# Performance work log

Hardware: AMD Instinct MI355X
Metric: run time of the kernel (lower is better)

## Reference

```python
import jax, jax.numpy as jnp
import numpy as np

NUM_LAYERS = 24
LN_EPS = 1e-5


def setup_inputs() -> dict:
    key = jax.random.key(0)
    ks = jax.random.split(key, 8)
    B, S = 256, 8192
    x = jax.random.uniform(ks[0], (B, S, 5), dtype=jnp.float32)
    # per-layer LayerNorm(4) params (torch default init: weight=1, bias=0; use
    # randomized values so the gather is non-trivial)
    ln_w = 1.0 + 0.1 * jax.random.normal(ks[1], (NUM_LAYERS, 4), dtype=jnp.float32)
    ln_b = 0.1 * jax.random.normal(ks[2], (NUM_LAYERS, 4), dtype=jnp.float32)
    # MLP 5 -> 64 -> 32 -> 1 (dropout inactive in eval mode)
    W1 = jax.random.normal(ks[3], (64, 5), dtype=jnp.float32) / np.sqrt(5)
    b1 = jnp.zeros((64,), dtype=jnp.float32)
    W2 = jax.random.normal(ks[4], (32, 64), dtype=jnp.float32) / np.sqrt(64)
    b2 = jnp.zeros((32,), dtype=jnp.float32)
    W3 = jax.random.normal(ks[5], (1, 32), dtype=jnp.float32) / np.sqrt(32)
    b3 = jnp.zeros((1,), dtype=jnp.float32)
    return {"x": x, "ln_w": ln_w, "ln_b": ln_b, "W1": W1, "b1": b1,
            "W2": W2, "b2": b2, "W3": W3, "b3": b3}


def reference(x, ln_w, ln_b, W1, b1, W2, b2, W3, b3):
    B, S, _ = x.shape
    x_flat = x.reshape(-1, 5)                      # [N, 5]
    layer_pos = x_flat[:, -1]                      # [N]
    layer_ids = jnp.clip((layer_pos * NUM_LAYERS).astype(jnp.int32), 0, NUM_LAYERS - 1)
    feats = x_flat[:, :4]                          # [N, 4]
    # vectorized per-token LayerNorm: gather per-token gamma/beta by layer id
    mean = jnp.mean(feats, axis=-1, keepdims=True)
    var = jnp.mean(jnp.square(feats - mean), axis=-1, keepdims=True)  # biased, as torch LN
    normed = (feats - mean) * jax.lax.rsqrt(var + LN_EPS)
    normed = normed * ln_w[layer_ids] + ln_b[layer_ids]               # [N, 4]
    x_norm = jnp.concatenate([normed, layer_pos[:, None]], axis=1)    # [N, 5]
    h = jax.nn.relu(x_norm @ W1.T + b1)            # [N, 64]
    h = jax.nn.relu(h @ W2.T + b2)                 # [N, 32]
    scores = h @ W3.T + b3                         # [N, 1]
    return scores.reshape(B, S)
```

## Files before the change

### kernel.cpp

```cpp
#include <hip/hip_runtime.h>
#include <stdint.h>

#define NUM_LAYERS 24
#define LN_EPS 1e-5f
#define N_ROWS (256 * 8192)
#define ROWS_PER_ITER 128
#define NUM_ITERS (N_ROWS / ROWS_PER_ITER)
#define NUM_BLOCKS 2048

typedef __attribute__((ext_vector_type(4)))  uint32_t u32x4;
typedef __attribute__((ext_vector_type(16))) float    f32x16;
typedef __attribute__((ext_vector_type(2)))  float    f32x2;
typedef __attribute__((ext_vector_type(2)))  __fp16   h16x2;

__device__ __forceinline__ uint32_t pk_f16_rtz(float lo, float hi) {
    h16x2 v = __builtin_amdgcn_cvt_pkrtz(lo, hi);
    uint32_t u; __builtin_memcpy(&u, &v, 4);
    return u;
}
__device__ __forceinline__ uint32_t pk_f16_rne(float lo, float hi) {
    __fp16 a = (__fp16)lo, b = (__fp16)hi;
    uint16_t ua, ub;
    __builtin_memcpy(&ua, &a, 2); __builtin_memcpy(&ub, &b, 2);
    return (uint32_t)ua | ((uint32_t)ub << 16);
}
__device__ __forceinline__ uint32_t pk_relu_f16(uint32_t d) {
    h16x2 v; __builtin_memcpy(&v, &d, 4);
    h16x2 z = {(__fp16)0.0f, (__fp16)0.0f};
    v = __builtin_elementwise_max(v, z);
    uint32_t u; __builtin_memcpy(&u, &v, 4);
    return u;
}

__device__ __forceinline__ u32x4 make_frag(uint32_t d0, uint32_t d1,
                                           uint32_t d2, uint32_t d3) {
    u32x4 f; f.x = d0; f.y = d1; f.z = d2; f.w = d3;
    return f;
}

__device__ __forceinline__ void mfma_l1(f32x16& d0, f32x16& d1,
                                        f32x16& d2, f32x16& d3,
                                        const u32x4& a0, const u32x4& a1,
                                        const u32x4& b0, const u32x4& b1) {
    asm("s_nop 2\n\t"
        "v_mfma_f32_32x32x16_f16 %0, %4, %6, 0\n\t"
        "v_mfma_f32_32x32x16_f16 %1, %5, %6, 0\n\t"
        "v_mfma_f32_32x32x16_f16 %2, %4, %7, 0\n\t"
        "v_mfma_f32_32x32x16_f16 %3, %5, %7, 0"
        : "=&v"(d0), "=&v"(d1), "=&v"(d2), "=&v"(d3)
        : "v"(a0), "v"(a1), "v"(b0), "v"(b1));
}
__device__ __forceinline__ void mfma_l2(f32x16& c0, f32x16& c1, const f32x16& cinit,
                                        const u32x4& w0, const u32x4& w1,
                                        const u32x4& w2, const u32x4& w3,
                                        const u32x4& h00, const u32x4& h01,
                                        const u32x4& h02, const u32x4& h03,
                                        const u32x4& h10, const u32x4& h11,
                                        const u32x4& h12, const u32x4& h13) {
    asm("s_nop 2\n\t"
        "v_mfma_f32_32x32x16_f16 %0, %3, %7, %2\n\t"
        "v_mfma_f32_32x32x16_f16 %1, %3, %11, %2\n\t"
        "v_mfma_f32_32x32x16_f16 %0, %4, %8, %0\n\t"
        "v_mfma_f32_32x32x16_f16 %1, %4, %12, %1\n\t"
        "v_mfma_f32_32x32x16_f16 %0, %5, %9, %0\n\t"
        "v_mfma_f32_32x32x16_f16 %1, %5, %13, %1\n\t"
        "v_mfma_f32_32x32x16_f16 %0, %6, %10, %0\n\t"
        "v_mfma_f32_32x32x16_f16 %1, %6, %14, %1"
        : "=&v"(c0), "=&v"(c1)
        : "v"(cinit), "v"(w0), "v"(w1), "v"(w2), "v"(w3),
          "v"(h00), "v"(h01), "v"(h02), "v"(h03),
          "v"(h10), "v"(h11), "v"(h12), "v"(h13));
}
__device__ __forceinline__ void mfma_fence2(f32x16& c0, f32x16& c1) {
    asm volatile("s_nop 7\n\ts_nop 7\n\ts_nop 7" : "+v"(c0), "+v"(c1));
}
__device__ __forceinline__ void mfma_fence4(f32x16& c0, f32x16& c1,
                                            f32x16& c2, f32x16& c3) {
    asm volatile("s_nop 7\n\ts_nop 7\n\ts_nop 7"
                 : "+v"(c0), "+v"(c1), "+v"(c2), "+v"(c3));
}

__device__ __forceinline__ int sigma_k(int p) {
    int hh = (p >> 2) & 1;
    int base = (p & 31) - 4 * hh;
    int r = (base & 3) + 4 * (base >> 3);
    return 32 * (p >> 5) + 16 * (r >> 3) + 8 * hh + (r & 7);
}

__global__ __launch_bounds__(256, 3) void router_mfma(
    const float* __restrict__ x,
    const float* __restrict__ ln_w,
    const float* __restrict__ ln_b,
    const float* __restrict__ W1,
    const float* __restrict__ b1,
    const float* __restrict__ W2,
    const float* __restrict__ b2,
    const float* __restrict__ W3,
    const float* __restrict__ b3,
    float* __restrict__ out)
{
    __shared__ uint32_t s_a1[2 * 64 * 4];
    __shared__ uint32_t s_w2[4 * 64 * 4];
    __shared__ float    s_w3[8 * 64 * 2];
    __shared__ float    s_b2[8 * 64 * 2];
    __shared__ float    s_ln[8 * NUM_LAYERS];

    const int t = threadIdx.x;

    if (t < 8 * NUM_LAYERS) {
        const int q = t & 7, lid = t >> 3;
        s_ln[q * NUM_LAYERS + lid] =
            (q < 4) ? ln_w[lid * 4 + q] : ln_b[lid * 4 + (q - 4)];
    }
    if (t < 128) {
        const int mt = t >> 6, ln = t & 63;
        const int n32l = ln & 31, hl = ln >> 5;
        uint32_t d0 = 0, d1 = 0, d2 = 0;
        if (!hl) {
            const int k = sigma_k(mt * 32 + n32l);
            d0 = pk_f16_rne(W1[k * 5 + 0], W1[k * 5 + 1]);
            d1 = pk_f16_rne(W1[k * 5 + 2], W1[k * 5 + 3]);
            d2 = pk_f16_rne(W1[k * 5 + 4], b1[k]);
        }
        uint32_t* p = &s_a1[(mt * 64 + ln) * 4];
        p[0] = d0; p[1] = d1; p[2] = d2; p[3] = 0;
    }
    {
        const int kt = t >> 6, ln = t & 63;
        const int n32l = ln & 31, hl = ln >> 5;
        const float* wp = W2 + n32l * 64 + kt * 16 + hl * 8;
        const float4 lo = *(const float4*)(wp);
        const float4 hi = *(const float4*)(wp + 4);
        uint32_t* p = &s_w2[(kt * 64 + ln) * 4];
        p[0] = pk_f16_rne(lo.x, lo.y);
        p[1] = pk_f16_rne(lo.z, lo.w);
        p[2] = pk_f16_rne(hi.x, hi.y);
        p[3] = pk_f16_rne(hi.z, hi.w);
    }
#pragma unroll
    for (int e = t; e < 512; e += 256) {
        const int r2 = e >> 6, ln = e & 63;
        const int hl = ln >> 5;
        const int n = ((2 * r2) & 3) + 8 * (r2 >> 1) + 4 * hl;
        s_w3[e * 2 + 0] = W3[n];
        s_w3[e * 2 + 1] = W3[n + 1];
        s_b2[e * 2 + 0] = b2[n];
        s_b2[e * 2 + 1] = b2[n + 1];
    }
    __syncthreads();

    const int lane = t & 63;
    const int wid  = t >> 6;
    const int h    = lane >> 5;

    u32x4 a1f[2], w2f[4];
#pragma unroll
    for (int mt = 0; mt < 2; ++mt)
        a1f[mt] = *(const u32x4*)&s_a1[(mt * 64 + lane) * 4];
#pragma unroll
    for (int kt = 0; kt < 4; ++kt)
        w2f[kt] = *(const u32x4*)&s_w2[(kt * 64 + lane) * 4];

    f32x16 c2init;
    f32x2 w3p[8];
#pragma unroll
    for (int r2 = 0; r2 < 8; ++r2) {
        w3p[r2] = *(const f32x2*)&s_w3[(r2 * 64 + lane) * 2];
        const f32x2 bp = *(const f32x2*)&s_b2[(r2 * 64 + lane) * 2];
        c2init[2 * r2]     = bp.x;
        c2init[2 * r2 + 1] = bp.y;
    }
    const float b3v = b3[0];
    const f32x2 z2 = {0.0f, 0.0f};

    const int total_waves = NUM_BLOCKS * 4;
    const int w = blockIdx.x * 4 + wid;

    int it = w;
    {
        const float* p0 = x + (size_t)(it * ROWS_PER_ITER + lane) * 5;
        const float* p1 = x + (size_t)(it * ROWS_PER_ITER + 64 + lane) * 5;
        float4 c40 = *(const float4*)p0; float cl0 = p0[4];
        float4 c41 = *(const float4*)p1; float cl1 = p1[4];

        while (true) {
            const int nit = it + total_waves;
            const bool more = nit < NUM_ITERS;
            const size_t nb = (size_t)(more ? nit : it) * ROWS_PER_ITER;
            const float* n0 = x + (nb + lane) * 5;
            const float* n1 = x + (nb + 64 + lane) * 5;
            const float4 nv40 = *(const float4*)n0; const float nl0 = n0[4];
            const float4 nv41 = *(const float4*)n1; const float nl1 = n1[4];

            const int rowBase = it * ROWS_PER_ITER;

#pragma unroll
            for (int grp = 0; grp < 2; ++grp) {
                const float4 cv = grp ? c41 : c40;
                const float  cl = grp ? cl1 : cl0;
                const int gbase = rowBase + 64 * grp;

                int lid = (int)(cl * (float)NUM_LAYERS);
                lid = lid < 0 ? 0 : (lid > NUM_LAYERS - 1 ? NUM_LAYERS - 1 : lid);

                const float m  = (cv.x + cv.y + cv.z + cv.w) * 0.25f;
                const float d0 = cv.x - m, d1 = cv.y - m,
                            d2 = cv.z - m, d3 = cv.w - m;
                const float var = (d0 * d0 + d1 * d1 + d2 * d2 + d3 * d3) * 0.25f;
                const float r   = rsqrtf(var + LN_EPS);

                const float xn0 = fmaf(d0, r * s_ln[0 * 24 + lid], s_ln[4 * 24 + lid]);
                const float xn1 = fmaf(d1, r * s_ln[1 * 24 + lid], s_ln[5 * 24 + lid]);
                const float xn2 = fmaf(d2, r * s_ln[2 * 24 + lid], s_ln[6 * 24 + lid]);
                const float xn3 = fmaf(d3, r * s_ln[3 * 24 + lid], s_ln[7 * 24 + lid]);

                const uint32_t e0 = pk_f16_rtz(xn0, xn1);
                const uint32_t e1 = pk_f16_rtz(xn2, xn3);
                const uint32_t e2 = pk_f16_rtz(cl, 1.0f);
                const uint32_t x0 = __shfl_xor((int)e0, 32, 64);
                const uint32_t x1 = __shfl_xor((int)e1, 32, 64);
                const uint32_t x2 = __shfl_xor((int)e2, 32, 64);

                const u32x4 bf_t0 = make_frag(e0, e1, e2, 0u);
                const u32x4 bf_t1 = make_frag(x0, x1, x2, 0u);

                f32x16 c1a0, c1b0, c1a1, c1b1;
                mfma_l1(c1a0, c1b0, c1a1, c1b1, a1f[0], a1f[1], bf_t0, bf_t1);
                mfma_fence4(c1a0, c1b0, c1a1, c1b1);

                u32x4 h1f0[4], h1f1[4];
#pragma unroll
                for (int kt = 0; kt < 4; ++kt) {
                    const f32x16& c1 = (kt < 2) ? c1a0 : c1b0;
                    const int roff = 8 * (kt & 1);
                    uint32_t dw[4];
#pragma unroll
                    for (int d = 0; d < 4; ++d)
                        dw[d] = pk_relu_f16(
                            pk_f16_rtz(c1[roff + 2 * d], c1[roff + 2 * d + 1]));
                    h1f0[kt] = make_frag(dw[0], dw[1], dw[2], dw[3]);
                }
#pragma unroll
                for (int kt = 0; kt < 4; ++kt) {
                    const f32x16& c1 = (kt < 2) ? c1a1 : c1b1;
                    const int roff = 8 * (kt & 1);
                    uint32_t dw[4];
#pragma unroll
                    for (int d = 0; d < 4; ++d)
                        dw[d] = pk_relu_f16(
                            pk_f16_rtz(c1[roff + 2 * d], c1[roff + 2 * d + 1]));
                    h1f1[kt] = make_frag(dw[0], dw[1], dw[2], dw[3]);
                }

                f32x16 c2_0, c2_1;
                mfma_l2(c2_0, c2_1, c2init,
                        w2f[0], w2f[1], w2f[2], w2f[3],
                        h1f0[0], h1f0[1], h1f0[2], h1f0[3],
                        h1f1[0], h1f1[1], h1f1[2], h1f1[3]);
                mfma_fence2(c2_0, c2_1);

                f32x2 acc0 = z2, acc1 = z2;
#pragma unroll
                for (int r2 = 0; r2 < 8; ++r2) {
                    f32x2 v0 = {c2_0[2 * r2], c2_0[2 * r2 + 1]};
                    f32x2 v1 = {c2_1[2 * r2], c2_1[2 * r2 + 1]};
                    v0 = __builtin_elementwise_max(v0, z2);
                    v1 = __builtin_elementwise_max(v1, z2);
                    acc0 = v0 * w3p[r2] + acc0;
                    acc1 = v1 * w3p[r2] + acc1;
                }
                float q0 = acc0.x + acc0.y;
                float q1 = acc1.x + acc1.y;
                q0 += __shfl_xor(q0, 32, 64);
                q1 += __shfl_xor(q1, 32, 64);

                out[gbase + lane] = (h ? q1 : q0) + b3v;
            }

            if (!more) break;
            it = nit;
            c40 = nv40; cl0 = nl0; c41 = nv41; cl1 = nl1;
        }
    }
}

extern "C" void kernel_launch(void* const* d_in, const int* in_sizes, int n_in,
                              void* d_out, int out_size, void* d_ws, size_t ws_size,
                              hipStream_t stream) {
    const float* x    = (const float*)d_in[0];
    const float* ln_w = (const float*)d_in[1];
    const float* ln_b = (const float*)d_in[2];
    const float* W1   = (const float*)d_in[3];
    const float* b1   = (const float*)d_in[4];
    const float* W2   = (const float*)d_in[5];
    const float* b2   = (const float*)d_in[6];
    const float* W3   = (const float*)d_in[7];
    const float* b3   = (const float*)d_in[8];
    float* out = (float*)d_out;

    router_mfma<<<NUM_BLOCKS, 256, 0, stream>>>(x, ln_w, ln_b, W1, b1, W2, b2,
                                                W3, b3, out);
}
```

Baseline: 107.2 us.

## Replace persistent prefetch loop with one-shot 256-row-per-wave batched processing

Drops the grid-stride loop that prefetched the next 128-row tile. Each wave now handles exactly 256 rows: it issues all four 64-row loads up front, runs LayerNorm and fragment packing for all four groups, then runs the MFMA chain per group. Launch bounds fall from 3 to 2 blocks per CU to allow the extra registers this needs. More memory-level parallelism per wave comes at the cost of lower occupancy and no overlap across tiles.

After: 106.6 us. About the same (-0.5%).

```diff
diff --git a/kernel.cpp b/kernel.cpp
--- a/kernel.cpp
+++ b/kernel.cpp
@@ -4,8 +4,6 @@
 #define NUM_LAYERS 24
 #define LN_EPS 1e-5f
 #define N_ROWS (256 * 8192)
-#define ROWS_PER_ITER 128
-#define NUM_ITERS (N_ROWS / ROWS_PER_ITER)
 #define NUM_BLOCKS 2048
 
 typedef __attribute__((ext_vector_type(4)))  uint32_t u32x4;
@@ -87,7 +85,7 @@
     return 32 * (p >> 5) + 16 * (r >> 3) + 8 * hh + (r & 7);
 }
 
-__global__ __launch_bounds__(256, 3) void router_mfma(
+__global__ __launch_bounds__(256, 2) void router_mfma(
     const float* __restrict__ x,
     const float* __restrict__ ln_w,
     const float* __restrict__ ln_b,
@@ -173,114 +171,101 @@
     const float b3v = b3[0];
     const f32x2 z2 = {0.0f, 0.0f};
 
-    const int total_waves = NUM_BLOCKS * 4;
     const int w = blockIdx.x * 4 + wid;
-
-    int it = w;
-    {
-        const float* p0 = x + (size_t)(it * ROWS_PER_ITER + lane) * 5;
-        const float* p1 = x + (size_t)(it * ROWS_PER_ITER + 64 + lane) * 5;
-        float4 c40 = *(const float4*)p0; float cl0 = p0[4];
-        float4 c41 = *(const float4*)p1; float cl1 = p1[4];
-
-        while (true) {
-            const int nit = it + total_waves;
-            const bool more = nit < NUM_ITERS;
-            const size_t nb = (size_t)(more ? nit : it) * ROWS_PER_ITER;
-            const float* n0 = x + (nb + lane) * 5;
-            const float* n1 = x + (nb + 64 + lane) * 5;
-            const float4 nv40 = *(const float4*)n0; const float nl0 = n0[4];
-            const float4 nv41 = *(const float4*)n1; const float nl1 = n1[4];
-
-            const int rowBase = it * ROWS_PER_ITER;
-
-#pragma unroll
-            for (int grp = 0; grp < 2; ++grp) {
-                const float4 cv = grp ? c41 : c40;
-                const float  cl = grp ? cl1 : cl0;
-                const int gbase = rowBase + 64 * grp;
-
-                int lid = (int)(cl * (float)NUM_LAYERS);
-                lid = lid < 0 ? 0 : (lid > NUM_LAYERS - 1 ? NUM_LAYERS - 1 : lid);
-
-                const float m  = (cv.x + cv.y + cv.z + cv.w) * 0.25f;
-                const float d0 = cv.x - m, d1 = cv.y - m,
-                            d2 = cv.z - m, d3 = cv.w - m;
-                const float var = (d0 * d0 + d1 * d1 + d2 * d2 + d3 * d3) * 0.25f;
-                const float r   = rsqrtf(var + LN_EPS);
-
-                const float xn0 = fmaf(d0, r * s_ln[0 * 24 + lid], s_ln[4 * 24 + lid]);
-                const float xn1 = fmaf(d1, r * s_ln[1 * 24 + lid], s_ln[5 * 24 + lid]);
-                const float xn2 = fmaf(d2, r * s_ln[2 * 24 + lid], s_ln[6 * 24 + lid]);
-                const float xn3 = fmaf(d3, r * s_ln[3 * 24 + lid], s_ln[7 * 24 + lid]);
-
-                const uint32_t e0 = pk_f16_rtz(xn0, xn1);
-                const uint32_t e1 = pk_f16_rtz(xn2, xn3);
-                const uint32_t e2 = pk_f16_rtz(cl, 1.0f);
-                const uint32_t x0 = __shfl_xor((int)e0, 32, 64);
-                const uint32_t x1 = __shfl_xor((int)e1, 32, 64);
-                const uint32_t x2 = __shfl_xor((int)e2, 32, 64);
-
-                const u32x4 bf_t0 = make_frag(e0, e1, e2, 0u);
-                const u32x4 bf_t1 = make_frag(x0, x1, x2, 0u);
-
-                f32x16 c1a0, c1b0, c1a1, c1b1;
-                mfma_l1(c1a0, c1b0, c1a1, c1b1, a1f[0], a1f[1], bf_t0, bf_t1);
-                mfma_fence4(c1a0, c1b0, c1a1, c1b1);
-
-                u32x4 h1f0[4], h1f1[4];
-#pragma unroll
-                for (int kt = 0; kt < 4; ++kt) {
-                    const f32x16& c1 = (kt < 2) ? c1a0 : c1b0;
-                    const int roff = 8 * (kt & 1);
-                    uint32_t dw[4];
-#pragma unroll
-                    for (int d = 0; d < 4; ++d)
-                        dw[d] = pk_relu_f16(
-                            pk_f16_rtz(c1[roff + 2 * d], c1[roff + 2 * d + 1]));
-                    h1f0[kt] = make_frag(dw[0], dw[1], dw[2], dw[3]);
-                }
-#pragma unroll
-                for (int kt = 0; kt < 4; ++kt) {
-                    const f32x16& c1 = (kt < 2) ? c1a1 : c1b1;
-                    const int roff = 8 * (kt & 1);
-                    uint32_t dw[4];
-#pragma unroll
-                    for (int d = 0; d < 4; ++d)
-                        dw[d] = pk_relu_f16(
-                            pk_f16_rtz(c1[roff + 2 * d], c1[roff + 2 * d + 1]));
-                    h1f1[kt] = make_frag(dw[0], dw[1], dw[2], dw[3]);
-                }
-
-                f32x16 c2_0, c2_1;
-                mfma_l2(c2_0, c2_1, c2init,
-                        w2f[0], w2f[1], w2f[2], w2f[3],
-                        h1f0[0], h1f0[1], h1f0[2], h1f0[3],
-                        h1f1[0], h1f1[1], h1f1[2], h1f1[3]);
-                mfma_fence2(c2_0, c2_1);
-
-                f32x2 acc0 = z2, acc1 = z2;
-#pragma unroll
-                for (int r2 = 0; r2 < 8; ++r2) {
-                    f32x2 v0 = {c2_0[2 * r2], c2_0[2 * r2 + 1]};
-                    f32x2 v1 = {c2_1[2 * r2], c2_1[2 * r2 + 1]};
-                    v0 = __builtin_elementwise_max(v0, z2);
-                    v1 = __builtin_elementwise_max(v1, z2);
-                    acc0 = v0 * w3p[r2] + acc0;
-                    acc1 = v1 * w3p[r2] + acc1;
-                }
-                float q0 = acc0.x + acc0.y;
-                float q1 = acc1.x + acc1.y;
-                q0 += __shfl_xor(q0, 32, 64);
-                q1 += __shfl_xor(q1, 32, 64);
-
-                out[gbase + lane] = (h ? q1 : q0) + b3v;
-            }
-
-            if (!more) break;
-            it = nit;
-            c40 = nv40; cl0 = nl0; c41 = nv41; cl1 = nl1;
-        }
+    const size_t rowBase = (size_t)w * 256;
+
+    float4 cv[4];
+    float  cl[4];
+#pragma unroll
+    for (int g = 0; g < 4; ++g) {
+        const float* p = x + (rowBase + 64 * g + lane) * 5;
+        cv[g] = *(const float4*)p;
+        cl[g] = p[4];
+    }
+
+    u32x4 bft[4][2];
+#pragma unroll
+    for (int g = 0; g < 4; ++g) {
+        int lid = (int)(cl[g] * (float)NUM_LAYERS);
+        lid = lid < 0 ? 0 : (lid > NUM_LAYERS - 1 ? NUM_LAYERS - 1 : lid);
+
+        const float m  = (cv[g].x + cv[g].y + cv[g].z + cv[g].w) * 0.25f;
+        const float d0 = cv[g].x - m, d1 = cv[g].y - m,
+                    d2 = cv[g].z - m, d3 = cv[g].w - m;
+        const float var = (d0 * d0 + d1 * d1 + d2 * d2 + d3 * d3) * 0.25f;
+        const float r   = rsqrtf(var + LN_EPS);
+
+        const float xn0 = fmaf(d0, r * s_ln[0 * 24 + lid], s_ln[4 * 24 + lid]);
+        const float xn1 = fmaf(d1, r * s_ln[1 * 24 + lid], s_ln[5 * 24 + lid]);
+        const float xn2 = fmaf(d2, r * s_ln[2 * 24 + lid], s_ln[6 * 24 + lid]);
+        const float xn3 = fmaf(d3, r * s_ln[3 * 24 + lid], s_ln[7 * 24 + lid]);
+
+        const uint32_t e0 = pk_f16_rtz(xn0, xn1);
+        const uint32_t e1 = pk_f16_rtz(xn2, xn3);
+        const uint32_t e2 = pk_f16_rtz(cl[g], 1.0f);
+        const uint32_t x0 = __shfl_xor((int)e0, 32, 64);
+        const uint32_t x1 = __shfl_xor((int)e1, 32, 64);
+        const uint32_t x2 = __shfl_xor((int)e2, 32, 64);
+
+        bft[g][0] = make_frag(e0, e1, e2, 0u);
+        bft[g][1] = make_frag(x0, x1, x2, 0u);
+    }
+
+#pragma unroll
+    for (int g = 0; g < 4; ++g) {
+        const size_t gbase = rowBase + 64 * g;
+
+        f32x16 c1a0, c1b0, c1a1, c1b1;
+        mfma_l1(c1a0, c1b0, c1a1, c1b1, a1f[0], a1f[1], bft[g][0], bft[g][1]);
+        mfma_fence4(c1a0, c1b0, c1a1, c1b1);
+
+        u32x4 h1f0[4], h1f1[4];
+#pragma unroll
+        for (int kt = 0; kt < 4; ++kt) {
+            const f32x16& c1 = (kt < 2) ? c1a0 : c1b0;
+            const int roff = 8 * (kt & 1);
+            uint32_t dw[4];
+#pragma unroll
+            for (int d = 0; d < 4; ++d)
+                dw[d] = pk_relu_f16(
+                    pk_f16_rtz(c1[roff + 2 * d], c1[roff + 2 * d + 1]));
+            h1f0[kt] = make_frag(dw[0], dw[1], dw[2], dw[3]);
+        }
+#pragma unroll
+        for (int kt = 0; kt < 4; ++kt) {
+            const f32x16& c1 = (kt < 2) ? c1a1 : c1b1;
+            const int roff = 8 * (kt & 1);
+            uint32_t dw[4];
+#pragma unroll
+            for (int d = 0; d < 4; ++d)
+                dw[d] = pk_relu_f16(
+                    pk_f16_rtz(c1[roff + 2 * d], c1[roff + 2 * d + 1]));
+            h1f1[kt] = make_frag(dw[0], dw[1], dw[2], dw[3]);
+        }
+
+        f32x16 c2_0, c2_1;
+        mfma_l2(c2_0, c2_1, c2init,
+                w2f[0], w2f[1], w2f[2], w2f[3],
+                h1f0[0], h1f0[1], h1f0[2], h1f0[3],
+                h1f1[0], h1f1[1], h1f1[2], h1f1[3]);
+        mfma_fence2(c2_0, c2_1);
+
+        f32x2 acc0 = z2, acc1 = z2;
+#pragma unroll
+        for (int r2 = 0; r2 < 8; ++r2) {
+            f32x2 v0 = {c2_0[2 * r2], c2_0[2 * r2 + 1]};
+            f32x2 v1 = {c2_1[2 * r2], c2_1[2 * r2 + 1]};
+            v0 = __builtin_elementwise_max(v0, z2);
+            v1 = __builtin_elementwise_max(v1, z2);
+            acc0 = v0 * w3p[r2] + acc0;
+            acc1 = v1 * w3p[r2] + acc1;
+        }
+        float q0 = acc0.x + acc0.y;
+        float q1 = acc1.x + acc1.y;
+        q0 += __shfl_xor(q0, 32, 64);
+        q1 += __shfl_xor(q1, 32, 64);
+
+        out[gbase + lane] = (h ? q1 : q0) + b3v;
     }
 }
 
```
